# Optimization experiments

Hardware: AMD Instinct MI355X
Metric: run time of the kernel (lower is better)

The kernel has to match this reference:

```python
import jax, jax.numpy as jnp
import numpy as np

C = 512          # channels
G = 32           # GroupNorm groups (flax default)
H = 8            # num_heads
EPS = 1e-6       # GroupNorm epsilon (flax default)
SPATIAL = (64, 64)


def setup_inputs() -> dict:
    key = jax.random.key(0)
    k1, k2 = jax.random.split(key)
    x = jax.random.normal(k1, SPATIAL + (C,), dtype=jnp.float32)
    gn_scale = jnp.ones((C,), dtype=jnp.float32)
    gn_bias = jnp.zeros((C,), dtype=jnp.float32)
    w_qkv = jax.random.normal(k2, (C, 3 * C), dtype=jnp.float32) / np.sqrt(C)
    b_qkv = jnp.zeros((3 * C,), dtype=jnp.float32)
    return {"x": x, "gn_scale": gn_scale, "gn_bias": gn_bias,
            "w_qkv": w_qkv, "b_qkv": b_qkv}


def reference(x, gn_scale, gn_bias, w_qkv, b_qkv):
    spatial_shape = x.shape[:-1]
    T = int(np.prod(spatial_shape))
    xf = x.reshape(T, C)

    # GroupNorm over (all spatial positions, channels within group) per group
    xg = xf.reshape(T, G, C // G)
    mean = jnp.mean(xg, axis=(0, 2), keepdims=True)
    var = jnp.var(xg, axis=(0, 2), keepdims=True)
    xn = ((xg - mean) * jax.lax.rsqrt(var + EPS)).reshape(T, C)
    xn = xn * gn_scale + gn_bias

    # QKV projection; note strided split: reshape (T, 3C) -> (T, C, 3)
    qkv = (xn @ w_qkv + b_qkv).reshape(T, C, 3)
    q, k, v = qkv[..., 0], qkv[..., 1], qkv[..., 2]

    ch = C // H
    scale = 1.0 / np.sqrt(np.sqrt(ch))
    qh = (q * scale).reshape(T, H, ch)
    kh = (k * scale).reshape(T, H, ch)
    vh = v.reshape(T, H, ch)

    w = jnp.einsum('thc,shc->ths', qh, kh)      # (T, H, T) attention scores
    w = jax.nn.softmax(w, axis=-1)
    a = jnp.einsum('ths,shc->thc', w, vh)       # (T, H, ch)
    return a.reshape(spatial_shape + (C,))
```

## Files before the change

kernel.cpp:

```cpp
#include <hip/hip_runtime.h>
#include <hip/hip_bf16.h>
#include <stdint.h>

typedef __attribute__((ext_vector_type(8))) short bf16x8;
typedef __attribute__((ext_vector_type(4))) float f32x4;
typedef __attribute__((ext_vector_type(16))) float f32x16;
typedef unsigned short u16;
typedef unsigned int u32;

constexpr int T  = 4096;
constexpr int C  = 512;
constexpr int H  = 8;
constexpr int CH = 64;
constexpr float EPS = 1e-6f;
constexpr float QKS   = 0.35355339059327378f;
constexpr float QKS_Q = 0.35355339059327378f * 1.4426950408889634f;

__device__ __forceinline__ float bf2f(u16 u) {
    union { unsigned int i; float f; } v; v.i = ((unsigned int)u) << 16; return v.f;
}
__device__ __forceinline__ u16 f2bf(float f) {
    union { float f; unsigned int i; } v; v.f = f;
    return (u16)((v.i + 0x7FFFu + ((v.i >> 16) & 1u)) >> 16);
}
__device__ __forceinline__ u32 pk2bf(float a, float b) {
    __hip_bfloat162 h = __float22bfloat162_rn(make_float2(a, b));
    u32 r; __builtin_memcpy(&r, &h, 4); return r;
}
__device__ __forceinline__ float ldin(const void* p, int i, int f32) {
    return f32 ? ((const float*)p)[i] : bf2f(((const u16*)p)[i]);
}
__device__ __forceinline__ void async16(const void* g, void* l) {
    __builtin_amdgcn_global_load_lds(
        (const __attribute__((address_space(1))) void*)g,
        (__attribute__((address_space(3))) void*)l,
        16, 0, 0);
}
__device__ __forceinline__ u32 pktrunc(float a, float b) {
    u32 ua = __float_as_uint(a), ub = __float_as_uint(b);
    return __builtin_amdgcn_perm(ub, ua, 0x07060302u);
}

__global__ void k_stats1(const void* x, float* gs2, int* flag) {
    int b = blockIdx.x, tid = threadIdx.x;
    int lane = tid & 63, w = tid >> 6;
    __shared__ int cnt;
    __shared__ float red[4][32][2];
    if (tid == 0) cnt = 0;
    __syncthreads();
    const u16* u = (const u16*)x;
    int huge = 0;
    for (int i = tid; i < 1024; i += 256) {
        float a = fabsf(bf2f(u[i]));
        if (!(a < 1e4f)) huge++;
    }
    if (huge) atomicAdd(&cnt, huge);
    __syncthreads();
    int f32 = (cnt >= 8) ? 1 : 0;
    if (b == 0 && tid == 0) *flag = f32;
    float s1 = 0.f, s2 = 0.f;
    if (f32) {
        const float4* xp = (const float4*)x + b * 4096;
        #pragma unroll
        for (int i = 0; i < 16; i++) {
            float4 v = xp[i * 256 + tid];
            s1 += (v.x + v.y) + (v.z + v.w);
            s2 += (v.x*v.x + v.y*v.y) + (v.z*v.z + v.w*v.w);
        }
        s1 += __shfl_xor(s1, 1); s2 += __shfl_xor(s2, 1);
        s1 += __shfl_xor(s1, 2); s2 += __shfl_xor(s2, 2);
        if ((lane & 3) == 0) {
            int gl = (lane >> 2) + 16 * (w & 1);
            red[w][gl][0] = s1; red[w][gl][1] = s2;
        }
        __syncthreads();
        if (tid < 32) {
            int g = tid, w0 = (g < 16) ? 0 : 1;
            gs2[b * 64 + g * 2]     = red[w0][g][0] + red[w0 + 2][g][0];
            gs2[b * 64 + g * 2 + 1] = red[w0][g][1] + red[w0 + 2][g][1];
        }
    } else {
        const uint4* xp = (const uint4*)x + b * 2048;
        #pragma unroll
        for (int i = 0; i < 8; i++) {
            uint4 v = xp[i * 256 + tid];
            float f[8] = { bf2f((u16)(v.x&0xffff)), bf2f((u16)(v.x>>16)),
                           bf2f((u16)(v.y&0xffff)), bf2f((u16)(v.y>>16)),
                           bf2f((u16)(v.z&0xffff)), bf2f((u16)(v.z>>16)),
                           bf2f((u16)(v.w&0xffff)), bf2f((u16)(v.w>>16)) };
            #pragma unroll
            for (int j = 0; j < 8; j++) { s1 += f[j]; s2 += f[j]*f[j]; }
        }
        s1 += __shfl_xor(s1, 1); s2 += __shfl_xor(s2, 1);
        if ((lane & 1) == 0) { red[w][lane >> 1][0] = s1; red[w][lane >> 1][1] = s2; }
        __syncthreads();
        if (tid < 32) {
            int g = tid;
            gs2[b * 64 + g * 2]     = red[0][g][0]+red[1][g][0]+red[2][g][0]+red[3][g][0];
            gs2[b * 64 + g * 2 + 1] = red[0][g][1]+red[1][g][1]+red[2][g][1]+red[3][g][1];
        }
    }
}

__global__ void k_fuse(const void* x, const float* __restrict__ gs2,
                       const void* gsc, const void* gbi, const void* wq,
                       u16* __restrict__ xn, u16* __restrict__ wt,
                       const int* __restrict__ flag) {
    int bx = blockIdx.x, tid = threadIdx.x;
    int f32 = *flag;
    if (bx < 1024) {
        __shared__ float sred[64];
        if (tid < 64) {
            float a0 = 0.f, a1 = 0.f, a2 = 0.f, a3 = 0.f;
            const float* p = gs2 + tid;
            #pragma unroll
            for (int b = 0; b < 32; b++) {
                a0 += p[(4*b + 0) * 64];
                a1 += p[(4*b + 1) * 64];
                a2 += p[(4*b + 2) * 64];
                a3 += p[(4*b + 3) * 64];
            }
            sred[tid] = (a0 + a1) + (a2 + a3);
        }
        __syncthreads();
        int idx = (bx * 256 + tid) * 8;
        int c = idx & (C - 1);
        int g = c >> 4;
        float mean = sred[2 * g] * (1.0f / 65536.0f);
        float var  = sred[2 * g + 1] * (1.0f / 65536.0f) - mean * mean;
        float rstd = rsqrtf(var + EPS);
        float v[8];
        if (f32) {
            float4 x0 = *(const float4*)((const float*)x + idx);
            float4 x1 = *(const float4*)((const float*)x + idx + 4);
            v[0]=x0.x; v[1]=x0.y; v[2]=x0.z; v[3]=x0.w;
            v[4]=x1.x; v[5]=x1.y; v[6]=x1.z; v[7]=x1.w;
        } else {
            uint4 u = *(const uint4*)((const u16*)x + idx);
            v[0]=bf2f((u16)(u.x&0xffff)); v[1]=bf2f((u16)(u.x>>16));
            v[2]=bf2f((u16)(u.y&0xffff)); v[3]=bf2f((u16)(u.y>>16));
            v[4]=bf2f((u16)(u.z&0xffff)); v[5]=bf2f((u16)(u.z>>16));
            v[6]=bf2f((u16)(u.w&0xffff)); v[7]=bf2f((u16)(u.w>>16));
        }
        float r[8];
        #pragma unroll
        for (int i = 0; i < 8; i++) {
            float a = rstd * ldin(gsc, c + i, f32);
            r[i] = v[i] * a + (ldin(gbi, c + i, f32) - mean * a);
        }
        uint4 o;
        o.x = pk2bf(r[0], r[1]); o.y = pk2bf(r[2], r[3]);
        o.z = pk2bf(r[4], r[5]); o.w = pk2bf(r[6], r[7]);
        *(uint4*)(xn + idx) = o;
    } else {
        __shared__ u16 Wl[48][64];
        int b = bx - 1024;
        int k0 = (b >> 5) * 64, c0 = (b & 31) * 48;
        #pragma unroll
        for (int it = 0; it < 3; it++) {
            int u_ = it * 256 + tid;
            int r = u_ / 12, cu = u_ % 12;
            int gi = (k0 + r) * 1536 + c0 + cu * 4;
            float v0, v1, v2, v3;
            if (f32) {
                float4 t4 = *(const float4*)((const float*)wq + gi);
                v0 = t4.x; v1 = t4.y; v2 = t4.z; v3 = t4.w;
            } else {
                uint2 t2 = *(const uint2*)((const u16*)wq + gi);
                v0 = bf2f((u16)(t2.x & 0xffff)); v1 = bf2f((u16)(t2.x >> 16));
                v2 = bf2f((u16)(t2.y & 0xffff)); v3 = bf2f((u16)(t2.y >> 16));
            }
            Wl[cu*4+0][r] = f2bf(v0); Wl[cu*4+1][r] = f2bf(v1);
            Wl[cu*4+2][r] = f2bf(v2); Wl[cu*4+3][r] = f2bf(v3);
        }
        __syncthreads();
        #pragma unroll
        for (int it = 0; it < 2; it++) {
            int u_ = it * 256 + tid;
            if (u_ < 384) {
                int mrow = u_ >> 3, kc = u_ & 7;
                int j = mrow >> 4, cci = mrow & 15;
                int m = j * 512 + (c0 / 3) + cci;
                int cl = 3 * cci + j;
                uint4 val = *(const uint4*)&Wl[cl][kc * 8];
                *(uint4*)(wt + m * 512 + k0 + kc * 8) = val;
            }
        }
    }
}

__global__ __launch_bounds__(256) void k_gemm(
    const u16* __restrict__ xn, const u16* __restrict__ wt,
    const void* __restrict__ bq, const int* __restrict__ flag,
    u16* __restrict__ qh, u16* __restrict__ kh, u16* __restrict__ vt)
{
    __shared__ char smem[49152];
    u16* Al = (u16*)smem;
    u16* Bl = (u16*)(smem + 16384);
    int bx = blockIdx.x;
    int bm = bx & 63, bn = bx >> 6;
    int tid = threadIdx.x;
    int w = tid >> 6, lane = tid & 63, quad = lane >> 4, l15 = lane & 15;
    f32x4 acc[4][2] = {};
    const u16* Ag = xn + bm * 64 * 512;
    const u16* Bg = wt + bn * 128 * 512;

    #pragma unroll
    for (int i = 0; i < 2; i++) {
        int L = i * 256 + tid, row = L >> 3, cc = ((L & 7) ^ (row & 7)) * 8;
        async16(Ag + row * 512 + cc, (void*)(Al + L * 8));
    }
    #pragma unroll
    for (int i = 0; i < 4; i++) {
        int L = i * 256 + tid, row = L >> 3, cc = ((L & 7) ^ (row & 7)) * 8;
        async16(Bg + row * 512 + cc, (void*)(Bl + L * 8));
    }

    #pragma unroll
    for (int ki = 0; ki < 8; ki++) {
        __syncthreads();
        if (ki < 7) {
            int kn = (ki + 1) * 64;
            int bo = ((ki + 1) & 1);
            #pragma unroll
            for (int i = 0; i < 2; i++) {
                int L = i * 256 + tid, row = L >> 3, cc = ((L & 7) ^ (row & 7)) * 8;
                async16(Ag + row * 512 + kn + cc, (void*)(Al + bo * 4096 + L * 8));
            }
            #pragma unroll
            for (int i = 0; i < 4; i++) {
                int L = i * 256 + tid, row = L >> 3, cc = ((L & 7) ^ (row & 7)) * 8;
                async16(Bg + row * 512 + kn + cc, (void*)(Bl + bo * 8192 + L * 8));
            }
        }
        const u16* Ab = Al + (ki & 1) * 4096;
        const u16* Bb = Bl + (ki & 1) * 8192;
        #pragma unroll
        for (int kk = 0; kk < 2; kk++) {
            bf16x8 af[4], bfr[2];
            #pragma unroll
            for (int mi = 0; mi < 4; mi++) {
                int row = mi * 16 + l15;
                af[mi] = *(const bf16x8*)(Ab + row * 64 + (((kk * 4 + quad) ^ (row & 7)) * 8));
            }
            #pragma unroll
            for (int ni = 0; ni < 2; ni++) {
                int row = w * 32 + ni * 16 + l15;
                bfr[ni] = *(const bf16x8*)(Bb + row * 64 + (((kk * 4 + quad) ^ (row & 7)) * 8));
            }
            #pragma unroll
            for (int mi = 0; mi < 4; mi++)
                #pragma unroll
                for (int ni = 0; ni < 2; ni++)
                    acc[mi][ni] = __builtin_amdgcn_mfma_f32_16x16x32_bf16(
                        af[mi], bfr[ni], acc[mi][ni], 0, 0, 0);
        }
    }
    int f32 = *flag;
    int t_base = bm * 64;
    int j = bn >> 2;
    if (j < 2) {
        u16* dst = j ? kh : qh;
        float s = j ? QKS : QKS_Q;
        #pragma unroll
        for (int ni = 0; ni < 2; ni++) {
            int n = bn * 128 + w * 32 + ni * 16 + l15;
            int r = n & 511, hh = r >> 6, cc = r & 63;
            float bias = ldin(bq, 3 * r + j, f32);
            #pragma unroll
            for (int mi = 0; mi < 4; mi++) {
                int tq = t_base + mi * 16 + quad * 4;
                #pragma unroll
                for (int rg = 0; rg < 4; rg++)
                    dst[(hh * T + tq + rg) * CH + cc] = f2bf((acc[mi][ni][rg] + bias) * s);
            }
        }
    } else {
        __syncthreads();
        u16* Tt = (u16*)smem;
        u16* Tw = Tt + w * 2048;
        int rbase = (bn - 8) * 128 + w * 32;
        int hh = rbase >> 6;
        #pragma unroll
        for (int ni = 0; ni < 2; ni++) {
            int r = rbase + ni * 16 + l15;
            float bias = ldin(bq, 3 * (r & 511) + 2, f32);
            int rl = ni * 16 + l15;
            #pragma unroll
            for (int mi = 0; mi < 4; mi++) {
                uint2 pv;
                pv.x = pk2bf(acc[mi][ni][0] + bias, acc[mi][ni][1] + bias);
                pv.y = pk2bf(acc[mi][ni][2] + bias, acc[mi][ni][3] + bias);
                int cs = (mi * 2 + (quad >> 1)) ^ (rl & 7);
                *(uint2*)((u32*)Tw + rl * 32 + cs * 4 + (quad & 1) * 2) = pv;
            }
        }
        int cc_hi = (w & 1) * 32;
        #pragma unroll
        for (int rr = 0; rr < 4; rr++) {
            int rl = rr * 8 + (lane >> 3);
            int g = lane & 7;
            bf16x8 val = *(const bf16x8*)(Tw + rl * 64 + ((g ^ (rl & 7)) * 8));
            *(uint4*)(vt + (hh * CH + cc_hi + rl) * T + t_base + g * 8) = *(uint4*)&val;
        }
    }
}

__global__ __launch_bounds__(256, 4) void k_attn(
    const u16* __restrict__ qh, const u16* __restrict__ kh,
    const u16* __restrict__ vt, float* __restrict__ opart, float* __restrict__ ls)
{
    __shared__ char lds[32768];
    u16* K0 = (u16*)lds;
    u16* V0 = (u16*)(lds + 16384);
    int bx = blockIdx.x;
    int h = bx >> 7, qb = (bx >> 2) & 31, ks = bx & 3;
    int t0 = qb * 128;
    int tid = threadIdx.x;
    int w = tid >> 6, lane = tid & 63;
    int l31 = lane & 31, hi = lane >> 5;

    const u16* Kg = kh + (h * T + ks * 1024) * CH;
    const u16* Vg = vt + h * CH * T + ks * 1024;

    int L0 = tid,       r0 = L0 >> 3, c0 = ((L0 & 7) ^ (r0 & 7)) * 8;
    int L1 = 256 + tid, r1 = L1 >> 3, c1 = ((L1 & 7) ^ (r1 & 7)) * 8;
    const u16* kp0 = Kg + r0 * CH + c0;
    const u16* kp1 = Kg + r1 * CH + c1;
    const u16* vp0 = Vg + r0 * T + c0;
    const u16* vp1 = Vg + r1 * T + c1;

    int off[2][4];
    #pragma unroll
    for (int rt = 0; rt < 2; rt++)
        #pragma unroll
        for (int c = 0; c < 4; c++) {
            int row = rt * 32 + l31;
            off[rt][c] = row * 64 + (((2 * c + hi) ^ (row & 7)) * 8);
        }

    bf16x8 bq[4];
    {
        const u16* qrow = qh + (h * T + t0 + w * 32 + l31) * CH;
        #pragma unroll
        for (int ksi = 0; ksi < 4; ksi++)
            bq[ksi] = *(const bf16x8*)(qrow + ksi * 16 + hi * 8);
    }

    async16(kp0, (void*)(K0 + L0 * 8));
    async16(kp1, (void*)(K0 + L1 * 8));
    async16(vp0, (void*)(V0 + L0 * 8));
    async16(vp1, (void*)(V0 + L1 * 8));

    f32x16 o[2] = {};
    float lsum = 0.f;

    for (int kt = 0; kt < 16; kt++) {
        int par = (kt & 1) * 4096;
        const u16* Kc = K0 + par;
        const u16* Vc = V0 + par;
        __syncthreads();
        if (kt < 15) {
            int nx = ((kt + 1) & 1) * 4096;
            int ko = (kt + 1) * 64 * CH;
            int vo = (kt + 1) * 64;
            async16(kp0 + ko, (void*)(K0 + nx + L0 * 8));
            async16(kp1 + ko, (void*)(K0 + nx + L1 * 8));
            async16(vp0 + vo, (void*)(V0 + nx + L0 * 8));
            async16(vp1 + vo, (void*)(V0 + nx + L1 * 8));
        }
        f32x16 sa[2] = {};
        #pragma unroll
        for (int t = 0; t < 2; t++)
            #pragma unroll
            for (int ksi = 0; ksi < 4; ksi++) {
                bf16x8 aK = *(const bf16x8*)(Kc + off[t][ksi]);
                sa[t] = __builtin_amdgcn_mfma_f32_32x32x16_bf16(aK, bq[ksi], sa[t], 0, 0, 0);
            }
        u32 bp[4][4];
        #pragma unroll
        for (int t = 0; t < 2; t++) {
            u32 p[8], xch[8];
            float rs = 0.f;
            #pragma unroll
            for (int pi = 0; pi < 8; pi++) {
                float e0 = exp2f(sa[t][2 * pi]);
                float e1 = exp2f(sa[t][2 * pi + 1]);
                rs += e0 + e1;
                p[pi] = pktrunc(e0, e1);
            }
            lsum += rs;
            #pragma unroll
            for (int pi = 0; pi < 8; pi++) xch[pi] = (u32)__shfl_xor((int)p[pi], 32);
            #pragma unroll
            for (int k2 = 0; k2 < 2; k2++) {
                int kst = t * 2 + k2;
                bp[kst][0] = hi ? xch[4*k2+2] : p[4*k2+0];
                bp[kst][1] = hi ? xch[4*k2+3] : p[4*k2+1];
                bp[kst][2] = hi ? p[4*k2+2]   : xch[4*k2+0];
                bp[kst][3] = hi ? p[4*k2+3]   : xch[4*k2+1];
            }
        }
        #pragma unroll
        for (int dt = 0; dt < 2; dt++)
            #pragma unroll
            for (int kst = 0; kst < 4; kst++) {
                bf16x8 aV = *(const bf16x8*)(Vc + off[dt][kst]);
                bf16x8 bpv;
                __builtin_memcpy(&bpv, bp[kst], 16);
                o[dt] = __builtin_amdgcn_mfma_f32_32x32x16_bf16(aV, bpv, o[dt], 0, 0, 0);
            }
    }
    lsum += __shfl_xor(lsum, 32);

    __syncthreads();
    float* Sw = (float*)(lds + w * 6144);
    int qg = t0 + w * 32;
    int q2 = lane >> 1, half = lane & 1;
    #pragma unroll
    for (int dt = 0; dt < 2; dt++) {
        #pragma unroll
        for (int reg = 0; reg < 16; reg++) {
            int dl = (reg & 3) + 8 * (reg >> 2) + 4 * hi;
            Sw[l31 * 33 + dl] = o[dt][reg];
        }
        const float* src = Sw + q2 * 33 + half * 16;
        float* dst = opart + ((ks * 8 + h) * T + qg + q2) * 64 + dt * 32 + half * 16;
        #pragma unroll
        for (int i = 0; i < 4; i++)
            *(f32x4*)(dst + i * 4) = *(const f32x4*)(src + i * 4);
    }
    if (hi == 0) ls[(ks * 8 + h) * T + qg + l31] = lsum;
}

__global__ void k_fin(const float* __restrict__ opart, const float* __restrict__ ls,
                      void* __restrict__ out, const int* __restrict__ flag) {
    int idx = (blockIdx.x * 256 + threadIdx.x) * 8;
    int d0 = idx & 63;
    int ht = idx >> 6;
    int t = ht & (T - 1), h = ht >> 12;
    float inv = 1.0f / (ls[ht] + ls[32768 + ht] + ls[65536 + ht] + ls[98304 + ht]);
    float v[8] = {};
    #pragma unroll
    for (int ks = 0; ks < 4; ks++) {
        float4 a0 = *(const float4*)(opart + ks * 2097152 + idx);
        float4 a1 = *(const float4*)(opart + ks * 2097152 + idx + 4);
        v[0] += a0.x; v[1] += a0.y; v[2] += a0.z; v[3] += a0.w;
        v[4] += a1.x; v[5] += a1.y; v[6] += a1.z; v[7] += a1.w;
    }
    #pragma unroll
    for (int i = 0; i < 8; i++) v[i] *= inv;
    int gbase = t * C + h * CH + d0;
    if (*flag) {
        *(float4*)((float*)out + gbase)     = make_float4(v[0], v[1], v[2], v[3]);
        *(float4*)((float*)out + gbase + 4) = make_float4(v[4], v[5], v[6], v[7]);
    } else {
        uint4 o;
        o.x = pk2bf(v[0], v[1]); o.y = pk2bf(v[2], v[3]);
        o.z = pk2bf(v[4], v[5]); o.w = pk2bf(v[6], v[7]);
        *(uint4*)((u16*)out + gbase) = o;
    }
}

extern "C" void kernel_launch(void* const* d_in, const int* in_sizes, int n_in,
                              void* d_out, int out_size, void* d_ws, size_t ws_size,
                              hipStream_t stream) {
    const void* x   = d_in[0];
    const void* gsc = d_in[1];
    const void* gbi = d_in[2];
    const void* wq  = d_in[3];
    const void* bq  = d_in[4];
    char* ws = (char*)d_ws;
    int*   flag = (int*)ws;
    char* base = ws + 8192;
    u16* qh = (u16*)(base);
    u16* kh = (u16*)(base + 4194304);
    u16* vt = (u16*)(base + 8388608);
    u16* xn = (u16*)(base + 12582912);
    u16* wt = (u16*)(base + 16777216);
    float* opart = (float*)(base + 12582912);
    float* ls    = (float*)(base + 46137344);
    float* gs2   = (float*)(base + 46661632);

    hipLaunchKernelGGL(k_stats1, dim3(128),  dim3(256), 0, stream, x, gs2, flag);
    hipLaunchKernelGGL(k_fuse,   dim3(1280), dim3(256), 0, stream, x, gs2, gsc, gbi, wq, xn, wt, flag);
    hipLaunchKernelGGL(k_gemm,   dim3(768),  dim3(256), 0, stream, xn, wt, bq, flag, qh, kh, vt);
    hipLaunchKernelGGL(k_attn,   dim3(1024), dim3(256), 0, stream, qh, kh, vt, opart, ls);
    hipLaunchKernelGGL(k_fin,    dim3(1024), dim3(256), 0, stream, opart, ls, d_out, flag);
}
```

Before: 162.1 us.

## Fuse split-K finalize into attention via atomic ticket, drop P shuffle exchange

Removes the separate k_fin launch: each attention block increments a per-(head, query-block) atomic counter, and the last of the four split blocks sums the partials, normalizes and writes the output. The P-fragment cross-half shuffle is removed by writing exp values straight into the MFMA B operand layout. This relies on a different V-transpose store order in k_gemm, which now reads two 8-byte halves from LDS. A memset of the tick counters is added per launch. The intent is to cut launch overhead and the shuffle cost, at the price of a tail of serial reduction work inside the attention grid and an extra memset.

```diff
diff --git a/kernel.cpp b/kernel.cpp
--- a/kernel.cpp
+++ b/kernel.cpp
@@ -300,15 +300,21 @@
         for (int rr = 0; rr < 4; rr++) {
             int rl = rr * 8 + (lane >> 3);
             int g = lane & 7;
-            bf16x8 val = *(const bf16x8*)(Tw + rl * 64 + ((g ^ (rl & 7)) * 8));
-            *(uint4*)(vt + (hh * CH + cc_hi + rl) * T + t_base + g * 8) = *(uint4*)&val;
+            int cA = (g & ~1) ^ (rl & 7);
+            int cB = ((g & ~1) + 1) ^ (rl & 7);
+            int ofs = (g & 1) * 4;
+            uint2 a = *(const uint2*)(Tw + rl * 64 + cA * 8 + ofs);
+            uint2 b = *(const uint2*)(Tw + rl * 64 + cB * 8 + ofs);
+            *(uint4*)(vt + (hh * CH + cc_hi + rl) * T + t_base + g * 8) =
+                make_uint4(a.x, a.y, b.x, b.y);
         }
     }
 }
 
 __global__ __launch_bounds__(256, 4) void k_attn(
     const u16* __restrict__ qh, const u16* __restrict__ kh,
-    const u16* __restrict__ vt, float* __restrict__ opart, float* __restrict__ ls)
+    const u16* __restrict__ vt, float* __restrict__ opart, float* __restrict__ ls,
+    int* __restrict__ tick, void* __restrict__ out, const int* __restrict__ flag)
 {
     __shared__ char lds[32768];
     u16* K0 = (u16*)lds;
@@ -380,26 +386,15 @@
         u32 bp[4][4];
         #pragma unroll
         for (int t = 0; t < 2; t++) {
-            u32 p[8], xch[8];
             float rs = 0.f;
             #pragma unroll
             for (int pi = 0; pi < 8; pi++) {
                 float e0 = exp2f(sa[t][2 * pi]);
                 float e1 = exp2f(sa[t][2 * pi + 1]);
                 rs += e0 + e1;
-                p[pi] = pktrunc(e0, e1);
+                bp[2 * t + (pi >> 2)][pi & 3] = pktrunc(e0, e1);
             }
             lsum += rs;
-            #pragma unroll
-            for (int pi = 0; pi < 8; pi++) xch[pi] = (u32)__shfl_xor((int)p[pi], 32);
-            #pragma unroll
-            for (int k2 = 0; k2 < 2; k2++) {
-                int kst = t * 2 + k2;
-                bp[kst][0] = hi ? xch[4*k2+2] : p[4*k2+0];
-                bp[kst][1] = hi ? xch[4*k2+3] : p[4*k2+1];
-                bp[kst][2] = hi ? p[4*k2+2]   : xch[4*k2+0];
-                bp[kst][3] = hi ? p[4*k2+3]   : xch[4*k2+1];
-            }
         }
         #pragma unroll
         for (int dt = 0; dt < 2; dt++)
@@ -431,34 +426,32 @@
             *(f32x4*)(dst + i * 4) = *(const f32x4*)(src + i * 4);
     }
     if (hi == 0) ls[(ks * 8 + h) * T + qg + l31] = lsum;
-}
-
-__global__ void k_fin(const float* __restrict__ opart, const float* __restrict__ ls,
-                      void* __restrict__ out, const int* __restrict__ flag) {
-    int idx = (blockIdx.x * 256 + threadIdx.x) * 8;
-    int d0 = idx & 63;
-    int ht = idx >> 6;
-    int t = ht & (T - 1), h = ht >> 12;
+
+    __threadfence();
+    __shared__ int rank_s;
+    if (tid == 0) rank_s = atomicAdd(&tick[h * 32 + qb], 1);
+    __syncthreads();
+    if (rank_s != 3) return;
+    __threadfence();
+    int f32v = *flag;
+    int q = tid >> 1, dh = (tid & 1) * 32;
+    int ht = h * T + t0 + q;
     float inv = 1.0f / (ls[ht] + ls[32768 + ht] + ls[65536 + ht] + ls[98304 + ht]);
-    float v[8] = {};
-    #pragma unroll
-    for (int ks = 0; ks < 4; ks++) {
-        float4 a0 = *(const float4*)(opart + ks * 2097152 + idx);
-        float4 a1 = *(const float4*)(opart + ks * 2097152 + idx + 4);
-        v[0] += a0.x; v[1] += a0.y; v[2] += a0.z; v[3] += a0.w;
-        v[4] += a1.x; v[5] += a1.y; v[6] += a1.z; v[7] += a1.w;
-    }
-    #pragma unroll
-    for (int i = 0; i < 8; i++) v[i] *= inv;
-    int gbase = t * C + h * CH + d0;
-    if (*flag) {
-        *(float4*)((float*)out + gbase)     = make_float4(v[0], v[1], v[2], v[3]);
-        *(float4*)((float*)out + gbase + 4) = make_float4(v[4], v[5], v[6], v[7]);
-    } else {
-        uint4 o;
-        o.x = pk2bf(v[0], v[1]); o.y = pk2bf(v[2], v[3]);
-        o.z = pk2bf(v[4], v[5]); o.w = pk2bf(v[6], v[7]);
-        *(uint4*)((u16*)out + gbase) = o;
+    const float* s0 = opart + (size_t)ht * 64 + dh;
+    int gbase = (t0 + q) * C + h * CH + dh;
+    #pragma unroll
+    for (int i = 0; i < 8; i++) {
+        f32x4 v = *(const f32x4*)(s0 + i * 4);
+        v += *(const f32x4*)(s0 + 2097152 + i * 4);
+        v += *(const f32x4*)(s0 + 4194304 + i * 4);
+        v += *(const f32x4*)(s0 + 6291456 + i * 4);
+        v *= inv;
+        if (f32v) {
+            *(f32x4*)((float*)out + gbase + i * 4) = v;
+        } else {
+            *(uint2*)((u16*)out + gbase + i * 4) =
+                make_uint2(pk2bf(v[0], v[1]), pk2bf(v[2], v[3]));
+        }
     }
 }
 
@@ -481,10 +474,11 @@
     float* opart = (float*)(base + 12582912);
     float* ls    = (float*)(base + 46137344);
     float* gs2   = (float*)(base + 46661632);
-
+    int*   tick  = (int*)(base + 46694400);
+
+    hipMemsetAsync(tick, 0, 1024, stream);
     hipLaunchKernelGGL(k_stats1, dim3(128),  dim3(256), 0, stream, x, gs2, flag);
     hipLaunchKernelGGL(k_fuse,   dim3(1280), dim3(256), 0, stream, x, gs2, gsc, gbi, wq, xn, wt, flag);
     hipLaunchKernelGGL(k_gemm,   dim3(768),  dim3(256), 0, stream, xn, wt, bq, flag, qh, kh, vt);
-    hipLaunchKernelGGL(k_attn,   dim3(1024), dim3(256), 0, stream, qh, kh, vt, opart, ls);
-    hipLaunchKernelGGL(k_fin,    dim3(1024), dim3(256), 0, stream, opart, ls, d_out, flag);
-}
+    hipLaunchKernelGGL(k_attn,   dim3(1024), dim3(256), 0, stream, qh, kh, vt, opart, ls, tick, d_out, flag);
+}
```

Result: slower. 405.9 us (+150.4%).
